# Kernel optimization log

Measured on AMD Instinct MI355X. Metric: run time of the kernel, lower is better.

The kernel has to match this reference:

```python
import jax, jax.numpy as jnp
import numpy as np

N_EMBD = 1024
N_HEAD = 16

def setup_inputs() -> dict:
    key = jax.random.key(0)
    k1, k2, k3 = jax.random.split(key, 3)
    x = jax.random.normal(k1, (2, 2048, N_EMBD), dtype=jnp.float32)
    # torch Linear(n, 3n): y = x @ W_attn (we store transposed weight directly)
    w_attn = jax.random.normal(k2, (N_EMBD, 3 * N_EMBD), dtype=jnp.float32) * 0.02
    w_proj = jax.random.normal(k3, (N_EMBD, N_EMBD), dtype=jnp.float32) * 0.02
    return {"x": x, "w_attn": w_attn, "w_proj": w_proj}

def reference(x, w_attn, w_proj):
    B, S, E = x.shape
    H = N_HEAD
    D = E // H
    qkv = x @ w_attn  # [B, S, 3E]
    q, k, v = jnp.split(qkv, 3, axis=-1)
    # [B, H, S, D]
    q = q.reshape(B, S, H, D).transpose(0, 2, 1, 3)
    k = k.reshape(B, S, H, D).transpose(0, 2, 1, 3)
    v = v.reshape(B, S, H, D).transpose(0, 2, 1, 3)
    scale = 1.0 / jnp.sqrt(jnp.asarray(D, dtype=x.dtype))
    a = jnp.einsum('bhqd,bhkd->bhqk', q, k) * scale  # [B, H, S, S]
    causal = jnp.tril(jnp.ones((S, S), dtype=bool))
    a = jnp.where(causal, a, -jnp.inf)
    a = jax.nn.softmax(a, axis=-1)
    y = jnp.einsum('bhqk,bhkd->bhqd', a, v)  # [B, H, S, D]
    y = y.transpose(0, 2, 1, 3).reshape(B, S, E)
    return y @ w_proj
```

## Files before the change

kernel.cpp:

```cpp
#include <hip/hip_runtime.h>

#define DEVI __device__ __forceinline__

typedef short bf16x8 __attribute__((ext_vector_type(8)));
typedef float f32x4 __attribute__((ext_vector_type(4)));
typedef unsigned short u16;
typedef unsigned int u32;

static constexpr int Bn = 2, S = 2048, E = 1024, H = 16, D = 64;
static constexpr int Mrows = Bn * S;
static constexpr int N_QKV = 3 * E;

DEVI u16 f2b(float f) {
  union { float f; u32 u; } c; c.f = f;
  return (u16)((c.u + 0x7FFFu + ((c.u >> 16) & 1u)) >> 16);
}

DEVI bf16x8 ld8(const u16* p) {
  union { uint4 u; bf16x8 v; } c;
  c.u = *reinterpret_cast<const uint4*>(p);
  return c.v;
}

#define MFMA(a, b, c) __builtin_amdgcn_mfma_f32_16x16x32_bf16(a, b, c, 0, 0, 0)

#define G2L16(gptr, lptr) \
  __builtin_amdgcn_global_load_lds((const __attribute__((address_space(1))) void*)(gptr), \
                                   (__attribute__((address_space(3))) void*)(lptr), 16, 0, 0)

__global__ __launch_bounds__(256) void prep(const float* __restrict__ x,
                                            const float* __restrict__ w_attn,
                                            const float* __restrict__ w_proj,
                                            u16* __restrict__ xb, u16* __restrict__ wabT,
                                            u16* __restrict__ wpbT) {
  __shared__ float t[32][33];
  int blk = blockIdx.x, tid = threadIdx.x;
  if (blk >= 4096) {
    int i = (blk - 4096) * 256 + tid;
    float4 f = reinterpret_cast<const float4*>(x)[i];
    ushort4 u;
    u.x = f2b(f.x); u.y = f2b(f.y); u.z = f2b(f.z); u.w = f2b(f.w);
    reinterpret_cast<ushort4*>(xb)[i] = u;
    return;
  }
  const float* in; u16* out; int R, C, bx, by;
  if (blk < 3072) {
    in = w_attn; out = wabT; R = E; C = N_QKV;
    bx = (blk % 96) * 32; by = (blk / 96) * 32;
  } else {
    int q = blk - 3072;
    in = w_proj; out = wpbT; R = E; C = E;
    bx = (q % 32) * 32; by = (q / 32) * 32;
  }
  int tx = tid & 31, ty = tid >> 5;
#pragma unroll
  for (int k = 0; k < 32; k += 8)
    t[ty + k][tx] = in[(size_t)(by + ty + k) * C + bx + tx];
  __syncthreads();
#pragma unroll
  for (int k = 0; k < 32; k += 8)
    out[(size_t)(bx + ty + k) * R + by + tx] = f2b(t[tx][ty + k]);
}

__global__ __launch_bounds__(256) void gemm_qkv(const u16* __restrict__ A, const u16* __restrict__ BT,
                                                u16* __restrict__ Qb, u16* __restrict__ Kb,
                                                u16* __restrict__ VbT) {
  constexpr int K = 1024, BK = 64;
  __shared__ __align__(16) u16 As[128 * BK];
  __shared__ __align__(16) u16 Bs[64 * BK];
  int tid = threadIdx.x;
  int w = tid >> 6, lane = tid & 63, quad = lane >> 4, l15 = lane & 15;
  int m0 = blockIdx.x * 128, n0 = blockIdx.y * 64;
  int mw = (w >> 1) * 64, nw = (w & 1) * 32;
  const u16* Ab = A + (size_t)m0 * K;
  const u16* Bb = BT + (size_t)n0 * K;
  f32x4 acc[4][2] = {};
  for (int k0 = 0; k0 < K; k0 += BK) {
#pragma unroll
    for (int j = 0; j < 4; j++) {
      int L = j * 256 + tid;
      int row = L >> 3, cg = (L & 7) ^ (row & 7);
      G2L16(Ab + (size_t)row * K + k0 + cg * 8, (char*)As + L * 16);
    }
#pragma unroll
    for (int j = 0; j < 2; j++) {
      int L = j * 256 + tid;
      int row = L >> 3, cg = (L & 7) ^ (row & 7);
      G2L16(Bb + (size_t)row * K + k0 + cg * 8, (char*)Bs + L * 16);
    }
    __syncthreads();
#pragma unroll
    for (int kk = 0; kk < 2; kk++) {
      int sg = ((kk << 2) | quad) ^ (l15 & 7);
      bf16x8 a[4], b[2];
#pragma unroll
      for (int i = 0; i < 4; i++) a[i] = ld8(&As[(mw + i * 16 + l15) * BK + sg * 8]);
#pragma unroll
      for (int i = 0; i < 2; i++) b[i] = ld8(&Bs[(nw + i * 16 + l15) * BK + sg * 8]);
#pragma unroll
      for (int mb = 0; mb < 4; mb++)
#pragma unroll
        for (int nb = 0; nb < 2; nb++)
          acc[mb][nb] = MFMA(a[mb], b[nb], acc[mb][nb]);
    }
    __syncthreads();
  }
#pragma unroll
  for (int mb = 0; mb < 4; mb++) {
    int m = m0 + mw + mb * 16 + quad * 4;
    int b = m >> 11, s = m & 2047;
#pragma unroll
    for (int nb = 0; nb < 2; nb++) {
      int n = n0 + nw + nb * 16 + l15;
      int sec = n >> 10, e = n & 1023, h = e >> 6, d = e & 63;
      int bh = b * H + h;
      if (sec == 0) {
#pragma unroll
        for (int r = 0; r < 4; r++)
          Qb[((size_t)bh * S + s + r) * D + d] = f2b(acc[mb][nb][r] * 0.1803368801111244f);
      } else if (sec == 1) {
#pragma unroll
        for (int r = 0; r < 4; r++)
          Kb[((size_t)bh * S + s + r) * D + d] = f2b(acc[mb][nb][r]);
      } else {
        ushort4 v;
        v.x = f2b(acc[mb][nb][0]); v.y = f2b(acc[mb][nb][1]);
        v.z = f2b(acc[mb][nb][2]); v.w = f2b(acc[mb][nb][3]);
        *reinterpret_cast<ushort4*>(VbT + ((size_t)bh * D + d) * S + s) = v;
      }
    }
  }
}

__global__ __launch_bounds__(256, 3) void attn(const u16* __restrict__ Qb, const u16* __restrict__ Kb,
                                               const u16* __restrict__ VbT, u16* __restrict__ Yb) {
  __shared__ __align__(16) u16 Ks[128 * 64];
  __shared__ __align__(16) u16 Vs[64 * 128];
  __shared__ __align__(16) u32 Ps[4][16 * 68];
  int w = threadIdx.x >> 6, lane = threadIdx.x & 63, quad = lane >> 4, l15 = lane & 15;
  int bh = blockIdx.x & 31, p = blockIdx.x >> 5;
  int b = bh >> 4, h = bh & 15;
  int qtA = 31 - p, qtB = p;
  int ncA = (qtA + 2) >> 1, ncB = (qtB + 2) >> 1;

  const u16* Kbh = Kb + (size_t)bh * S * D;
  const u16* Vbh = VbT + (size_t)bh * D * S;
  u32* myP = &Ps[w][0];
  const u16* myP16 = (const u16*)myP;
  int prow = l15 * 68 + quad * 2;

  int qbA = qtA * 64 + w * 16, qbB = qtB * 64 + w * 16;
  int kmaxA = qbA + 16, kmaxB = qbB + 16;
  const u16* QpA = Qb + ((size_t)bh * S + qbA + l15) * D + quad * 8;
  const u16* QpB = Qb + ((size_t)bh * S + qbB + l15) * D + quad * 8;
  bf16x8 bqA0 = ld8(QpA), bqA1 = ld8(QpA + 32);
  bf16x8 bqB0 = ld8(QpB), bqB1 = ld8(QpB + 32);

  float lA = 0.f, lB = 0.f;
  f32x4 oA[4] = {}, oB[4] = {};
  int kbase = 0;

  auto process = [&](int q_base, int kmaxW, bf16x8 bq0, bf16x8 bq1, f32x4* o, float& lpart) {
#pragma unroll
    for (int mb = 0; mb < 8; mb++) {
      int kb = kbase + mb * 16;
      u32 pa = 0, pb = 0;
      if (kb < kmaxW) {
        int row = mb * 16 + l15;
        bf16x8 ak0 = ld8(&Ks[row * 64 + ((quad ^ (row & 7)) * 8)]);
        bf16x8 ak1 = ld8(&Ks[row * 64 + (((quad + 4) ^ (row & 7)) * 8)]);
        f32x4 z = {};
        z = MFMA(ak0, bq0, z);
        z = MFMA(ak1, bq1, z);
        if (kb == q_base) {
#pragma unroll
          for (int r = 0; r < 4; r++)
            if (quad * 4 + r > l15) z[r] = -1e30f;
        }
        float p0 = __builtin_amdgcn_exp2f(z[0]);
        float p1 = __builtin_amdgcn_exp2f(z[1]);
        float p2 = __builtin_amdgcn_exp2f(z[2]);
        float p3 = __builtin_amdgcn_exp2f(z[3]);
        lpart += (p0 + p1) + (p2 + p3);
        union { float f; u32 u; } c0, c1, c2, c3;
        c0.f = p0; c1.f = p1; c2.f = p2; c3.f = p3;
        pa = __builtin_amdgcn_perm(c1.u + 0x8000u, c0.u + 0x8000u, 0x07060302u);
        pb = __builtin_amdgcn_perm(c3.u + 0x8000u, c2.u + 0x8000u, 0x07060302u);
      }
      uint2 pw; pw.x = pa; pw.y = pb;
      *reinterpret_cast<uint2*>(&myP[prow + mb * 8]) = pw;
    }
#pragma unroll
    for (int ch = 0; ch < 4; ch++) {
      if (kbase + ch * 32 < kmaxW) {
        bf16x8 bp = ld8(myP16 + l15 * 136 + ch * 32 + quad * 8);
#pragma unroll
        for (int dd = 0; dd < 4; dd++) {
          int rv = dd * 16 + l15;
          bf16x8 av = ld8(&Vs[rv * 128 + (((ch * 4 + quad) ^ (rv & 15)) * 8)]);
          o[dd] = MFMA(av, bp, o[dd]);
        }
      }
    }
  };

  for (int c = 0; c < ncA; c++) {
    kbase = c * 128;
    __syncthreads();
    const u16* Kg = Kbh + (size_t)kbase * D;
#pragma unroll
    for (int j = 0; j < 4; j++) {
      int L = (w * 4 + j) * 64 + lane;
      int row = L >> 3, cg = (L & 7) ^ (row & 7);
      G2L16(Kg + (size_t)row * 64 + cg * 8, (char*)Ks + L * 16);
    }
    const u16* Vg = Vbh + kbase;
#pragma unroll
    for (int j = 0; j < 4; j++) {
      int L = (w * 4 + j) * 64 + lane;
      int row = L >> 4, cg = (L & 15) ^ (row & 15);
      G2L16(Vg + (size_t)row * S + cg * 8, (char*)Vs + L * 16);
    }
    __syncthreads();

    process(qbA, kmaxA, bqA0, bqA1, oA, lA);
    if (c < ncB)
      process(qbB, kmaxB, bqB0, bqB1, oB, lB);
  }

  {
    float l = lA; l += __shfl_xor(l, 16); l += __shfl_xor(l, 32);
    float rinv = 1.0f / l;
    u16* Yp = Yb + ((size_t)b * S + qbA + l15) * E + h * 64 + quad * 4;
#pragma unroll
    for (int dd = 0; dd < 4; dd++) {
      ushort4 y;
      y.x = f2b(oA[dd][0] * rinv); y.y = f2b(oA[dd][1] * rinv);
      y.z = f2b(oA[dd][2] * rinv); y.w = f2b(oA[dd][3] * rinv);
      *reinterpret_cast<ushort4*>(Yp + dd * 16) = y;
    }
  }
  {
    float l = lB; l += __shfl_xor(l, 16); l += __shfl_xor(l, 32);
    float rinv = 1.0f / l;
    u16* Yp = Yb + ((size_t)b * S + qbB + l15) * E + h * 64 + quad * 4;
#pragma unroll
    for (int dd = 0; dd < 4; dd++) {
      ushort4 y;
      y.x = f2b(oB[dd][0] * rinv); y.y = f2b(oB[dd][1] * rinv);
      y.z = f2b(oB[dd][2] * rinv); y.w = f2b(oB[dd][3] * rinv);
      *reinterpret_cast<ushort4*>(Yp + dd * 16) = y;
    }
  }
}

__global__ __launch_bounds__(256) void gemm_proj(const u16* __restrict__ A, const u16* __restrict__ BT,
                                                 float* __restrict__ out) {
  constexpr int K = 1024, BK = 64;
  __shared__ __align__(16) u16 As[128 * BK];
  __shared__ __align__(16) u16 Bs[64 * BK];
  int tid = threadIdx.x;
  int w = tid >> 6, lane = tid & 63, quad = lane >> 4, l15 = lane & 15;
  int m0 = blockIdx.x * 128, n0 = blockIdx.y * 64;
  int mw = (w >> 1) * 64, nw = (w & 1) * 32;
  const u16* Ab = A + (size_t)m0 * K;
  const u16* Bb = BT + (size_t)n0 * K;
  f32x4 acc[4][2] = {};
  for (int k0 = 0; k0 < K; k0 += BK) {
#pragma unroll
    for (int j = 0; j < 4; j++) {
      int L = j * 256 + tid;
      int row = L >> 3, cg = (L & 7) ^ (row & 7);
      G2L16(Ab + (size_t)row * K + k0 + cg * 8, (char*)As + L * 16);
    }
#pragma unroll
    for (int j = 0; j < 2; j++) {
      int L = j * 256 + tid;
      int row = L >> 3, cg = (L & 7) ^ (row & 7);
      G2L16(Bb + (size_t)row * K + k0 + cg * 8, (char*)Bs + L * 16);
    }
    __syncthreads();
#pragma unroll
    for (int kk = 0; kk < 2; kk++) {
      int sg = ((kk << 2) | quad) ^ (l15 & 7);
      bf16x8 a[4], b[2];
#pragma unroll
      for (int i = 0; i < 4; i++) a[i] = ld8(&As[(mw + i * 16 + l15) * BK + sg * 8]);
#pragma unroll
      for (int i = 0; i < 2; i++) b[i] = ld8(&Bs[(nw + i * 16 + l15) * BK + sg * 8]);
#pragma unroll
      for (int mb = 0; mb < 4; mb++)
#pragma unroll
        for (int nb = 0; nb < 2; nb++)
          acc[mb][nb] = MFMA(a[mb], b[nb], acc[mb][nb]);
    }
    __syncthreads();
  }
#pragma unroll
  for (int mb = 0; mb < 4; mb++) {
    int m = m0 + mw + mb * 16 + quad * 4;
#pragma unroll
    for (int nb = 0; nb < 2; nb++) {
      int n = n0 + nw + nb * 16 + l15;
#pragma unroll
      for (int r = 0; r < 4; r++)
        out[(size_t)(m + r) * E + n] = acc[mb][nb][r];
    }
  }
}

extern "C" void kernel_launch(void* const* d_in, const int* in_sizes, int n_in,
                              void* d_out, int out_size, void* d_ws, size_t ws_size,
                              hipStream_t stream) {
  const float* x = (const float*)d_in[0];
  const float* w_attn = (const float*)d_in[1];
  const float* w_proj = (const float*)d_in[2];
  float* out = (float*)d_out;
  char* ws = (char*)d_ws;

  u16* xb   = (u16*)(ws);
  u16* wabT = (u16*)(ws + 8388608);
  u16* wpbT = (u16*)(ws + 14680064);
  u16* Qb   = (u16*)(ws + 16777216);
  u16* Kb   = (u16*)(ws + 25165824);
  u16* VbT  = (u16*)(ws + 33554432);
  u16* Yb   = (u16*)(ws + 41943040);

  prep<<<8192, 256, 0, stream>>>(x, w_attn, w_proj, xb, wabT, wpbT);
  gemm_qkv<<<dim3(Mrows / 128, N_QKV / 64), 256, 0, stream>>>(xb, wabT, Qb, Kb, VbT);
  attn<<<Bn * H * (S / 128), 256, 0, stream>>>(Qb, Kb, VbT, Yb);
  gemm_proj<<<dim3(Mrows / 128, E / 64), 256, 0, stream>>>(Yb, wpbT, out);
}
```

Baseline: 172.7 us.

## Split paired causal query tiles into separate attention blocks

Each attention workgroup previously handled two 64-row query tiles (a long one and a short one, paired for balanced causal work) and shared the K/V loads between them. Now each workgroup handles a single query tile and the grid doubles, with the longest tiles scheduled first. This gives more parallelism and drops the duplicate register state, at the cost of loading K/V tiles separately per query tile and leaving the load balance to the hardware scheduler.

```diff
diff --git a/kernel.cpp b/kernel.cpp
--- a/kernel.cpp
+++ b/kernel.cpp
@@ -138,10 +138,9 @@
   __shared__ __align__(16) u16 Vs[64 * 128];
   __shared__ __align__(16) u32 Ps[4][16 * 68];
   int w = threadIdx.x >> 6, lane = threadIdx.x & 63, quad = lane >> 4, l15 = lane & 15;
-  int bh = blockIdx.x & 31, p = blockIdx.x >> 5;
+  int bh = blockIdx.x & 31, qt = 31 - (blockIdx.x >> 5);
   int b = bh >> 4, h = bh & 15;
-  int qtA = 31 - p, qtB = p;
-  int ncA = (qtA + 2) >> 1, ncB = (qtB + 2) >> 1;
+  int nc = (qt + 2) >> 1;
 
   const u16* Kbh = Kb + (size_t)bh * S * D;
   const u16* Vbh = VbT + (size_t)bh * D * S;
@@ -149,23 +148,40 @@
   const u16* myP16 = (const u16*)myP;
   int prow = l15 * 68 + quad * 2;
 
-  int qbA = qtA * 64 + w * 16, qbB = qtB * 64 + w * 16;
-  int kmaxA = qbA + 16, kmaxB = qbB + 16;
-  const u16* QpA = Qb + ((size_t)bh * S + qbA + l15) * D + quad * 8;
-  const u16* QpB = Qb + ((size_t)bh * S + qbB + l15) * D + quad * 8;
-  bf16x8 bqA0 = ld8(QpA), bqA1 = ld8(QpA + 32);
-  bf16x8 bqB0 = ld8(QpB), bqB1 = ld8(QpB + 32);
-
-  float lA = 0.f, lB = 0.f;
-  f32x4 oA[4] = {}, oB[4] = {};
-  int kbase = 0;
-
-  auto process = [&](int q_base, int kmaxW, bf16x8 bq0, bf16x8 bq1, f32x4* o, float& lpart) {
+  int q_base = qt * 64 + w * 16;
+  int qrow = q_base + l15;
+  int kmax = q_base + 16;
+
+  const u16* Qp = Qb + ((size_t)bh * S + qrow) * D + quad * 8;
+  bf16x8 bq0 = ld8(Qp), bq1 = ld8(Qp + 32);
+
+  float lpart = 0.f;
+  f32x4 o[4] = {};
+
+  for (int c = 0; c < nc; c++) {
+    int kbase = c * 128;
+    __syncthreads();
+    const u16* Kg = Kbh + (size_t)kbase * D;
+#pragma unroll
+    for (int j = 0; j < 4; j++) {
+      int L = (w * 4 + j) * 64 + lane;
+      int row = L >> 3, cg = (L & 7) ^ (row & 7);
+      G2L16(Kg + (size_t)row * 64 + cg * 8, (char*)Ks + L * 16);
+    }
+    const u16* Vg = Vbh + kbase;
+#pragma unroll
+    for (int j = 0; j < 4; j++) {
+      int L = (w * 4 + j) * 64 + lane;
+      int row = L >> 4, cg = (L & 15) ^ (row & 15);
+      G2L16(Vg + (size_t)row * S + cg * 8, (char*)Vs + L * 16);
+    }
+    __syncthreads();
+
 #pragma unroll
     for (int mb = 0; mb < 8; mb++) {
       int kb = kbase + mb * 16;
       u32 pa = 0, pb = 0;
-      if (kb < kmaxW) {
+      if (kb < kmax) {
         int row = mb * 16 + l15;
         bf16x8 ak0 = ld8(&Ks[row * 64 + ((quad ^ (row & 7)) * 8)]);
         bf16x8 ak1 = ld8(&Ks[row * 64 + (((quad + 4) ^ (row & 7)) * 8)]);
@@ -192,7 +208,7 @@
     }
 #pragma unroll
     for (int ch = 0; ch < 4; ch++) {
-      if (kbase + ch * 32 < kmaxW) {
+      if (kbase + ch * 32 < kmax) {
         bf16x8 bp = ld8(myP16 + l15 * 136 + ch * 32 + quad * 8);
 #pragma unroll
         for (int dd = 0; dd < 4; dd++) {
@@ -202,55 +218,19 @@
         }
       }
     }
-  };
-
-  for (int c = 0; c < ncA; c++) {
-    kbase = c * 128;
-    __syncthreads();
-    const u16* Kg = Kbh + (size_t)kbase * D;
-#pragma unroll
-    for (int j = 0; j < 4; j++) {
-      int L = (w * 4 + j) * 64 + lane;
-      int row = L >> 3, cg = (L & 7) ^ (row & 7);
-      G2L16(Kg + (size_t)row * 64 + cg * 8, (char*)Ks + L * 16);
-    }
-    const u16* Vg = Vbh + kbase;
-#pragma unroll
-    for (int j = 0; j < 4; j++) {
-      int L = (w * 4 + j) * 64 + lane;
-      int row = L >> 4, cg = (L & 15) ^ (row & 15);
-      G2L16(Vg + (size_t)row * S + cg * 8, (char*)Vs + L * 16);
-    }
-    __syncthreads();
-
-    process(qbA, kmaxA, bqA0, bqA1, oA, lA);
-    if (c < ncB)
-      process(qbB, kmaxB, bqB0, bqB1, oB, lB);
-  }
-
-  {
-    float l = lA; l += __shfl_xor(l, 16); l += __shfl_xor(l, 32);
-    float rinv = 1.0f / l;
-    u16* Yp = Yb + ((size_t)b * S + qbA + l15) * E + h * 64 + quad * 4;
-#pragma unroll
-    for (int dd = 0; dd < 4; dd++) {
-      ushort4 y;
-      y.x = f2b(oA[dd][0] * rinv); y.y = f2b(oA[dd][1] * rinv);
-      y.z = f2b(oA[dd][2] * rinv); y.w = f2b(oA[dd][3] * rinv);
-      *reinterpret_cast<ushort4*>(Yp + dd * 16) = y;
-    }
-  }
-  {
-    float l = lB; l += __shfl_xor(l, 16); l += __shfl_xor(l, 32);
-    float rinv = 1.0f / l;
-    u16* Yp = Yb + ((size_t)b * S + qbB + l15) * E + h * 64 + quad * 4;
-#pragma unroll
-    for (int dd = 0; dd < 4; dd++) {
-      ushort4 y;
-      y.x = f2b(oB[dd][0] * rinv); y.y = f2b(oB[dd][1] * rinv);
-      y.z = f2b(oB[dd][2] * rinv); y.w = f2b(oB[dd][3] * rinv);
-      *reinterpret_cast<ushort4*>(Yp + dd * 16) = y;
-    }
+  }
+
+  float l = lpart;
+  l += __shfl_xor(l, 16);
+  l += __shfl_xor(l, 32);
+  float rinv = 1.0f / l;
+  u16* Yp = Yb + ((size_t)b * S + qrow) * E + h * 64 + quad * 4;
+#pragma unroll
+  for (int dd = 0; dd < 4; dd++) {
+    ushort4 y;
+    y.x = f2b(o[dd][0] * rinv); y.y = f2b(o[dd][1] * rinv);
+    y.z = f2b(o[dd][2] * rinv); y.w = f2b(o[dd][3] * rinv);
+    *reinterpret_cast<ushort4*>(Yp + dd * 16) = y;
   }
 }
 
@@ -328,6 +308,6 @@
 
   prep<<<8192, 256, 0, stream>>>(x, w_attn, w_proj, xb, wabT, wpbT);
   gemm_qkv<<<dim3(Mrows / 128, N_QKV / 64), 256, 0, stream>>>(xb, wabT, Qb, Kb, VbT);
-  attn<<<Bn * H * (S / 128), 256, 0, stream>>>(Qb, Kb, VbT, Yb);
+  attn<<<Bn * H * (S / 64), 256, 0, stream>>>(Qb, Kb, VbT, Yb);
   gemm_proj<<<dim3(Mrows / 128, E / 64), 256, 0, stream>>>(Yb, wpbT, out);
 }
```

Result: faster. 166.6 us (-3.5%).
